# Optimization experiments

Measured on AMD Instinct MI355X. Metric: run time of the kernel, lower is better.

## Reference

```python
import jax, jax.numpy as jnp
import numpy as np

N_BITS = 8
LENGTH = 1 << N_BITS  # 256
BATCH = 131072


def fwht(x):
    """Fast Walsh-Hadamard transform along the last axis (natural ordering, unnormalized)."""
    L = x.shape[-1]
    h = 1
    while h < L:
        x = x.reshape(x.shape[:-1] + (L // (2 * h), 2, h))
        a = x[..., 0, :]
        b = x[..., 1, :]
        x = jnp.stack((a + b, a - b), axis=-2).reshape(x.shape[:-3] + (L,))
        h *= 2
    return x


def wh_transform(x):
    # Normalization depends on the share dimension size (dim -2), as in FFWHT.transform
    n_shares = x.shape[-2]
    return fwht(x) / (2.0 ** (N_BITS / n_shares / 2))


def convolve_wh(x):
    # x: (batch, n_shares, length)
    x_wh = wh_transform(x)                      # (B, S, L)
    prod = jnp.prod(x_wh, axis=1, keepdims=True)  # (B, 1, L)
    return wh_transform(prod)[:, 0, :]          # (B, L)


def setup_inputs() -> dict:
    key = jax.random.key(0)
    k0, k1, k2 = jax.random.split(key, 3)
    return {
        "beta_0": jax.random.normal(k0, (BATCH, LENGTH), dtype=jnp.float32),
        "beta_1": jax.random.normal(k1, (BATCH, LENGTH), dtype=jnp.float32),
        "masked_k": jax.random.normal(k2, (BATCH, LENGTH), dtype=jnp.float32),
    }


def reference(beta_0, beta_1, masked_k):
    # log-probas of every input leakage
    lp_beta_0 = jax.nn.log_softmax(beta_0, axis=-1)
    lp_beta_1 = jax.nn.log_softmax(beta_1, axis=-1)
    lp_masked = jax.nn.log_softmax(masked_k, axis=-1)
    # normalize_probs=False: raw leakages go into the group convolution
    p_beta = jnp.stack([beta_0, beta_1], axis=1)              # (B, 2, L)
    cat = jnp.concatenate([p_beta, masked_k[:, None, :]], 1)  # (B, 3, L)
    res = convolve_wh(cat)                                    # (B, L)
    lp_target = jax.nn.log_softmax(res, axis=-1)
    # log_probas dict: beta_0, beta_1, masked_k, target_k
    return (lp_beta_0, lp_beta_1, lp_masked, lp_target)
```

## Files before the change

kernel.cpp:

```cpp
#include <hip/hip_runtime.h>

#define LEN 256
#define ROWS_PER_BLOCK 4

__device__ __forceinline__ float wave_max(float v) {
#pragma unroll
    for (int m = 32; m >= 1; m >>= 1) v = fmaxf(v, __shfl_xor(v, m, 64));
    return v;
}

__device__ __forceinline__ float wave_sum(float v) {
#pragma unroll
    for (int m = 32; m >= 1; m >>= 1) v += __shfl_xor(v, m, 64);
    return v;
}

__device__ __forceinline__ void fwht256(float r[4], int lane) {
    float t0 = r[0] + r[1], t1 = r[0] - r[1];
    float t2 = r[2] + r[3], t3 = r[2] - r[3];
    r[0] = t0 + t2; r[1] = t1 + t3;
    r[2] = t0 - t2; r[3] = t1 - t3;
#pragma unroll
    for (int m = 1; m <= 32; m <<= 1) {
        float s = (lane & m) ? -1.0f : 1.0f;
#pragma unroll
        for (int j = 0; j < 4; ++j) {
            float other = __shfl_xor(r[j], m, 64);
            r[j] = fmaf(s, r[j], other);
        }
    }
}

__device__ __forceinline__ void log_softmax_store(const float v[4],
                                                  float* __restrict__ row_out,
                                                  int lane) {
    float mx = wave_max(fmaxf(fmaxf(v[0], v[1]), fmaxf(v[2], v[3])));
    float s = __expf(v[0] - mx) + __expf(v[1] - mx) +
              __expf(v[2] - mx) + __expf(v[3] - mx);
    s = wave_sum(s);
    float lse = mx + __logf(s);
    float4 o = make_float4(v[0] - lse, v[1] - lse, v[2] - lse, v[3] - lse);
    ((float4*)row_out)[lane] = o;
}

__global__ __launch_bounds__(256) void group_recombine_kernel(
        const float* __restrict__ b0, const float* __restrict__ b1,
        const float* __restrict__ mk, float* __restrict__ out, int rows) {
    const int wave = threadIdx.x >> 6;
    const int lane = threadIdx.x & 63;
    const int row = blockIdx.x * ROWS_PER_BLOCK + wave;
    if (row >= rows) return;

    const size_t base = (size_t)row * LEN;
    const size_t stride = (size_t)rows * LEN;

    float4 v = ((const float4*)(b0 + base))[lane];
    float a[4] = {v.x, v.y, v.z, v.w};
    float w0[4] = {a[0], a[1], a[2], a[3]};
    fwht256(w0, lane);
    log_softmax_store(a, out + base, lane);

    v = ((const float4*)(b1 + base))[lane];
    float b[4] = {v.x, v.y, v.z, v.w};
    float w1[4] = {b[0], b[1], b[2], b[3]};
    fwht256(w1, lane);
    log_softmax_store(b, out + stride + base, lane);

    v = ((const float4*)(mk + base))[lane];
    float c[4] = {v.x, v.y, v.z, v.w};
    float w2[4] = {c[0], c[1], c[2], c[3]};
    fwht256(w2, lane);
    log_softmax_store(c, out + 2 * stride + base, lane);

    float pr[4];
#pragma unroll
    for (int j = 0; j < 4; ++j) pr[j] = w0[j] * w1[j] * w2[j];
    fwht256(pr, lane);
#pragma unroll
    for (int j = 0; j < 4; ++j) pr[j] *= (1.0f / 256.0f);
    log_softmax_store(pr, out + 3 * stride + base, lane);
}

extern "C" void kernel_launch(void* const* d_in, const int* in_sizes, int n_in,
                              void* d_out, int out_size, void* d_ws, size_t ws_size,
                              hipStream_t stream) {
    const float* b0 = (const float*)d_in[0];
    const float* b1 = (const float*)d_in[1];
    const float* mk = (const float*)d_in[2];
    float* out = (float*)d_out;
    const int rows = in_sizes[0] / LEN;
    dim3 grid((rows + ROWS_PER_BLOCK - 1) / ROWS_PER_BLOCK);
    dim3 block(64 * ROWS_PER_BLOCK);
    group_recombine_kernel<<<grid, block, 0, stream>>>(b0, b1, mk, out, rows);
}
```

Measured before the change: 775.7 us.

## Process two rows per wave with eight elements per lane

Each 64-lane wave now handles two rows, one per 32-lane half, with each lane holding eight elements. More butterfly stages of the Walsh-Hadamard transform run in registers, and fewer cross-lane shuffles are needed per row and per reduction. All three input loads are issued up front to raise memory-level parallelism. In exchange each lane uses more registers and the grid has half as many waves.

```diff
diff --git a/kernel.cpp b/kernel.cpp
--- a/kernel.cpp
+++ b/kernel.cpp
@@ -1,46 +1,57 @@
 #include <hip/hip_runtime.h>
 
 #define LEN 256
-#define ROWS_PER_BLOCK 4
+#define WAVES_PER_BLOCK 4
+#define ROWS_PER_BLOCK (WAVES_PER_BLOCK * 2)
 
-__device__ __forceinline__ float wave_max(float v) {
+__device__ __forceinline__ float half_max(float v) {
 #pragma unroll
-    for (int m = 32; m >= 1; m >>= 1) v = fmaxf(v, __shfl_xor(v, m, 64));
+    for (int m = 16; m >= 1; m >>= 1) v = fmaxf(v, __shfl_xor(v, m, 64));
     return v;
 }
 
-__device__ __forceinline__ float wave_sum(float v) {
+__device__ __forceinline__ float half_sum(float v) {
 #pragma unroll
-    for (int m = 32; m >= 1; m >>= 1) v += __shfl_xor(v, m, 64);
+    for (int m = 16; m >= 1; m >>= 1) v += __shfl_xor(v, m, 64);
     return v;
 }
 
-__device__ __forceinline__ void fwht256(float r[4], int lane) {
+__device__ __forceinline__ void fwht256(float r[8], int sl) {
     float t0 = r[0] + r[1], t1 = r[0] - r[1];
     float t2 = r[2] + r[3], t3 = r[2] - r[3];
-    r[0] = t0 + t2; r[1] = t1 + t3;
-    r[2] = t0 - t2; r[3] = t1 - t3;
+    float t4 = r[4] + r[5], t5 = r[4] - r[5];
+    float t6 = r[6] + r[7], t7 = r[6] - r[7];
+    float u0 = t0 + t2, u1 = t1 + t3, u2 = t0 - t2, u3 = t1 - t3;
+    float u4 = t4 + t6, u5 = t5 + t7, u6 = t4 - t6, u7 = t5 - t7;
+    r[0] = u0 + u4; r[1] = u1 + u5; r[2] = u2 + u6; r[3] = u3 + u7;
+    r[4] = u0 - u4; r[5] = u1 - u5; r[6] = u2 - u6; r[7] = u3 - u7;
 #pragma unroll
-    for (int m = 1; m <= 32; m <<= 1) {
-        float s = (lane & m) ? -1.0f : 1.0f;
+    for (int m = 1; m <= 16; m <<= 1) {
+        float s = (sl & m) ? -1.0f : 1.0f;
 #pragma unroll
-        for (int j = 0; j < 4; ++j) {
-            float other = __shfl_xor(r[j], m, 64);
-            r[j] = fmaf(s, r[j], other);
+        for (int j = 0; j < 8; ++j) {
+            float o = __shfl_xor(r[j], m, 64);
+            r[j] = fmaf(s, r[j], o);
         }
     }
 }
 
-__device__ __forceinline__ void log_softmax_store(const float v[4],
+__device__ __forceinline__ void log_softmax_store(const float v[8],
                                                   float* __restrict__ row_out,
-                                                  int lane) {
-    float mx = wave_max(fmaxf(fmaxf(v[0], v[1]), fmaxf(v[2], v[3])));
-    float s = __expf(v[0] - mx) + __expf(v[1] - mx) +
-              __expf(v[2] - mx) + __expf(v[3] - mx);
-    s = wave_sum(s);
-    float lse = mx + __logf(s);
-    float4 o = make_float4(v[0] - lse, v[1] - lse, v[2] - lse, v[3] - lse);
-    ((float4*)row_out)[lane] = o;
+                                                  int sl) {
+    float mx = fmaxf(fmaxf(fmaxf(v[0], v[1]), fmaxf(v[2], v[3])),
+                     fmaxf(fmaxf(v[4], v[5]), fmaxf(v[6], v[7])));
+    mx = half_max(mx);
+    float d[8];
+    float s = 0.0f;
+#pragma unroll
+    for (int j = 0; j < 8; ++j) { d[j] = v[j] - mx; s += __expf(d[j]); }
+    s = half_sum(s);
+    float ls = __logf(s);
+    float4 o0 = make_float4(d[0] - ls, d[1] - ls, d[2] - ls, d[3] - ls);
+    float4 o1 = make_float4(d[4] - ls, d[5] - ls, d[6] - ls, d[7] - ls);
+    ((float4*)row_out)[sl] = o0;
+    ((float4*)row_out)[32 + sl] = o1;
 }
 
 __global__ __launch_bounds__(256) void group_recombine_kernel(
@@ -48,37 +59,40 @@
         const float* __restrict__ mk, float* __restrict__ out, int rows) {
     const int wave = threadIdx.x >> 6;
     const int lane = threadIdx.x & 63;
-    const int row = blockIdx.x * ROWS_PER_BLOCK + wave;
+    const int sl = lane & 31;
+    const int h = lane >> 5;
+    const int row = blockIdx.x * ROWS_PER_BLOCK + wave * 2 + h;
     if (row >= rows) return;
 
     const size_t base = (size_t)row * LEN;
     const size_t stride = (size_t)rows * LEN;
 
-    float4 v = ((const float4*)(b0 + base))[lane];
-    float a[4] = {v.x, v.y, v.z, v.w};
-    float w0[4] = {a[0], a[1], a[2], a[3]};
-    fwht256(w0, lane);
-    log_softmax_store(a, out + base, lane);
+    const float4* p0 = (const float4*)(b0 + base);
+    const float4* p1 = (const float4*)(b1 + base);
+    const float4* p2 = (const float4*)(mk + base);
+    float4 a0 = p0[sl], a1 = p0[32 + sl];
+    float4 c0 = p1[sl], c1 = p1[32 + sl];
+    float4 e0 = p2[sl], e1 = p2[32 + sl];
 
-    v = ((const float4*)(b1 + base))[lane];
-    float b[4] = {v.x, v.y, v.z, v.w};
-    float w1[4] = {b[0], b[1], b[2], b[3]};
-    fwht256(w1, lane);
-    log_softmax_store(b, out + stride + base, lane);
+    float w0[8] = {a0.x, a0.y, a0.z, a0.w, a1.x, a1.y, a1.z, a1.w};
+    log_softmax_store(w0, out + base, sl);
+    fwht256(w0, sl);
 
-    v = ((const float4*)(mk + base))[lane];
-    float c[4] = {v.x, v.y, v.z, v.w};
-    float w2[4] = {c[0], c[1], c[2], c[3]};
-    fwht256(w2, lane);
-    log_softmax_store(c, out + 2 * stride + base, lane);
+    float w1[8] = {c0.x, c0.y, c0.z, c0.w, c1.x, c1.y, c1.z, c1.w};
+    log_softmax_store(w1, out + stride + base, sl);
+    fwht256(w1, sl);
 
-    float pr[4];
+    float w2[8] = {e0.x, e0.y, e0.z, e0.w, e1.x, e1.y, e1.z, e1.w};
+    log_softmax_store(w2, out + 2 * stride + base, sl);
+    fwht256(w2, sl);
+
+    float pr[8];
 #pragma unroll
-    for (int j = 0; j < 4; ++j) pr[j] = w0[j] * w1[j] * w2[j];
-    fwht256(pr, lane);
+    for (int j = 0; j < 8; ++j) pr[j] = w0[j] * w1[j] * w2[j];
+    fwht256(pr, sl);
 #pragma unroll
-    for (int j = 0; j < 4; ++j) pr[j] *= (1.0f / 256.0f);
-    log_softmax_store(pr, out + 3 * stride + base, lane);
+    for (int j = 0; j < 8; ++j) pr[j] *= (1.0f / 256.0f);
+    log_softmax_store(pr, out + 3 * stride + base, sl);
 }
 
 extern "C" void kernel_launch(void* const* d_in, const int* in_sizes, int n_in,
@@ -90,6 +104,6 @@
     float* out = (float*)d_out;
     const int rows = in_sizes[0] / LEN;
     dim3 grid((rows + ROWS_PER_BLOCK - 1) / ROWS_PER_BLOCK);
-    dim3 block(64 * ROWS_PER_BLOCK);
+    dim3 block(64 * WAVES_PER_BLOCK);
     group_recombine_kernel<<<grid, block, 0, stream>>>(b0, b1, mk, out, rows);
 }
```

After: 770.5 us. Within noise of the previous version (-0.7%).
